# Kernel tuning notes

Measured on AMD Instinct MI355X. Metric: run time of the kernel, lower is better.

Reference implementation:

```python
import jax, jax.numpy as jnp
import numpy as np

N_HEADS = 8
D_MODEL = 256
HEAD_DEPTH = D_MODEL // N_HEADS
B, S = 2, 4096


def setup_inputs() -> dict:
    key = jax.random.key(0)
    ks = jax.random.split(key, 8)
    scale = 1.0 / np.sqrt(D_MODEL)
    return {
        "q": jax.random.normal(ks[0], (B, S, D_MODEL), dtype=jnp.float32),
        "k": jax.random.normal(ks[1], (B, S, D_MODEL), dtype=jnp.float32),
        "v": jax.random.normal(ks[2], (B, S, D_MODEL), dtype=jnp.float32),
        "mask": jax.random.randint(ks[3], (B, S, S), 0, 2).astype(jnp.bool_),
        "wq": jax.random.normal(ks[4], (D_MODEL, D_MODEL), dtype=jnp.float32) * scale,
        "wk": jax.random.normal(ks[5], (D_MODEL, D_MODEL), dtype=jnp.float32) * scale,
        "wv": jax.random.normal(ks[6], (D_MODEL, D_MODEL), dtype=jnp.float32) * scale,
        "w_out": jax.random.normal(ks[7], (D_MODEL, D_MODEL), dtype=jnp.float32) * scale,
    }


def _split_heads(x):
    # [B, S, D] -> [B, H, S, Dh]
    b, s, _ = x.shape
    return x.reshape(b, s, N_HEADS, HEAD_DEPTH).transpose(0, 2, 1, 3)


def reference(q, k, v, mask, wq, wk, wv, w_out):
    Q = _split_heads(q @ wq)
    K = _split_heads(k @ wk)
    V = _split_heads(v @ wv)
    # [B, H, Sq, Sk]
    scores = jnp.einsum('bhqd,bhkd->bhqk', Q, K) / jnp.sqrt(
        jnp.asarray(HEAD_DEPTH, dtype=Q.dtype))
    # mask True -> -inf, broadcast over heads
    scores = jnp.where(mask[:, None, :, :], -jnp.inf, scores)
    probs = jax.nn.softmax(scores, axis=-1)
    attn = jnp.einsum('bhqk,bhkd->bhqd', probs, V)
    attn = attn.transpose(0, 2, 1, 3).reshape(q.shape[0], -1, D_MODEL)
    return attn @ w_out
```

## Files before the change

### kernel.cpp

```cpp
#include <hip/hip_runtime.h>
#include <stdint.h>

typedef __bf16 bf16;
typedef __bf16 bf16x8 __attribute__((ext_vector_type(8)));
typedef __bf16 bf16x4 __attribute__((ext_vector_type(4)));
typedef float  f32x4  __attribute__((ext_vector_type(4)));
typedef float  f32x16 __attribute__((ext_vector_type(16)));
typedef float  float4v __attribute__((ext_vector_type(4)));
typedef unsigned int uint;
typedef unsigned long long ull;

#define QSCALE 0.25505003984214403f

__global__ __launch_bounds__(256) void transpose_w(
    const float* __restrict__ w0, const float* __restrict__ w1,
    const float* __restrict__ w2, const float* __restrict__ w3,
    bf16* __restrict__ WT) {
  const int wsel = blockIdx.z;
  const float* W = wsel == 0 ? w0 : wsel == 1 ? w1 : wsel == 2 ? w2 : w3;
  const int k0 = blockIdx.x * 64, n0 = blockIdx.y * 64;
  __shared__ __align__(16) bf16 t[64][72];
  const int tid = threadIdx.x;
  {
    const int kk = (tid >> 4) << 2;
    const int nn = (tid & 15) << 2;
#pragma unroll
    for (int r = 0; r < 4; ++r) {
      float4v a = *(const float4v*)(W + (size_t)(k0 + kk + r) * 256 + n0 + nn);
#pragma unroll
      for (int j = 0; j < 4; ++j) t[nn + j][kk + r] = (bf16)a[j];
    }
  }
  __syncthreads();
  {
    const int ni = tid >> 2;
    const int c  = (tid & 3) * 16;
    bf16x8 o0 = *(const bf16x8*)(&t[ni][c]);
    bf16x8 o1 = *(const bf16x8*)(&t[ni][c + 8]);
    bf16* dst = WT + (size_t)wsel * 65536 + (size_t)(n0 + ni) * 256 + k0 + c;
    *(bf16x8*)dst = o0;
    *(bf16x8*)(dst + 8) = o1;
  }
}

__global__ __launch_bounds__(256) void proj_pack(
    const float* __restrict__ xq, const float* __restrict__ xk, const float* __restrict__ xv,
    const bf16* __restrict__ WT,
    bf16* __restrict__ Qo, bf16* __restrict__ Ko, bf16* __restrict__ Vt,
    const int* __restrict__ mask, uint* __restrict__ M2) {
  const int tid = threadIdx.x;
  if (blockIdx.x >= 768) {
    const int pid = blockIdx.x - 768;
    const int wid = pid * 4 + (tid >> 6);
    const int lane = tid & 63;
    const int row = wid >> 2, chunk = wid & 3;
    const int b = row >> 12, q = row & 4095;
    const size_t base = (size_t)row * 4096 + chunk * 1024 + lane;
    ull bl[16];
#pragma unroll
    for (int j = 0; j < 16; ++j) bl[j] = __ballot(mask[base + 64 * j] != 0);
    if (lane == 0) {
      uint* o = M2 + (size_t)b * 524288 + q;
#pragma unroll
      for (int j = 0; j < 16; ++j) {
        const int kdw = chunk * 32 + 2 * j;
        o[(size_t)kdw * 4096] = (uint)bl[j];
        o[(size_t)(kdw + 1) * 4096] = (uint)(bl[j] >> 32);
      }
    }
    return;
  }
  const int z = blockIdx.x >> 8;
  const int r8 = blockIdx.x & 255;
  const int m0 = (r8 >> 1) * 64, n0 = (r8 & 1) * 128;
  const float* X = z == 0 ? xq : (z == 1 ? xk : xv);
  const bf16* wt = WT + (size_t)z * 65536;
  const int wave = tid >> 6, lane = tid & 63;
  const int nl = lane & 15, quad = lane >> 4;
  const int arow = m0 + wave * 16 + nl;
  const float* xrow = X + (size_t)arow * 256;

  f32x4 zero4 = {0.f, 0.f, 0.f, 0.f};
  f32x4 acc[8];
#pragma unroll
  for (int i = 0; i < 8; ++i) acc[i] = zero4;

  for (int ks = 0; ks < 8; ++ks) {
    float4v a0 = *(const float4v*)(xrow + ks * 32 + quad * 8);
    float4v a1 = *(const float4v*)(xrow + ks * 32 + quad * 8 + 4);
    bf16x8 af;
#pragma unroll
    for (int i = 0; i < 4; ++i) { af[i] = (bf16)a0[i]; af[4 + i] = (bf16)a1[i]; }
#pragma unroll
    for (int nf = 0; nf < 8; ++nf) {
      bf16x8 bfr = *(const bf16x8*)(wt + (size_t)(n0 + nf * 16 + nl) * 256 + ks * 32 + quad * 8);
      acc[nf] = __builtin_amdgcn_mfma_f32_16x16x32_bf16(af, bfr, acc[nf], 0, 0, 0);
    }
  }

  const int Rbase = m0 + wave * 16 + quad * 4;
  if (z == 2) {
    const int b = Rbase >> 12, s = Rbase & 4095;
#pragma unroll
    for (int nf = 0; nf < 8; ++nf) {
      const int col = n0 + nf * 16 + nl;
      const int h = col >> 5, d = col & 31;
      bf16x4 o;
#pragma unroll
      for (int rr = 0; rr < 4; ++rr) o[rr] = (bf16)acc[nf][rr];
      *(bf16x4*)(Vt + (((size_t)(b * 8 + h)) * 32 + d) * 4096 + s) = o;
    }
  } else {
    const float scale = (z == 0) ? QSCALE : 1.0f;
    bf16* Out = z == 0 ? Qo : Ko;
#pragma unroll
    for (int nf = 0; nf < 8; ++nf) {
      const int col = n0 + nf * 16 + nl;
      const int h = col >> 5, d = col & 31;
#pragma unroll
      for (int rr = 0; rr < 4; ++rr) {
        const int R = Rbase + rr;
        const int b = R >> 12, s = R & 4095;
        Out[(((size_t)(b * 8 + h)) * 4096 + s) * 32 + d] = (bf16)(acc[nf][rr] * scale);
      }
    }
  }
}

__global__ __launch_bounds__(256) void attn_kernel(
    const bf16* __restrict__ Qg, const bf16* __restrict__ Kg,
    const bf16* __restrict__ Vtg, const uint* __restrict__ M2,
    bf16* __restrict__ Og) {
  const int bh = blockIdx.y, b = bh >> 3, h = bh & 7;
  const int q0 = blockIdx.x * 64;
  const int tid = threadIdx.x, w = tid >> 6, lane = tid & 63;
  const int nl = lane & 31, half = lane >> 5;

  __shared__ float Ored[4][32][66];
  __shared__ float Lsum[64][8];

  bf16x8 qf[2][2];
  {
    const bf16* Qbase = Qg + ((size_t)bh * 4096 + q0) * 32;
#pragma unroll
    for (int qt = 0; qt < 2; ++qt)
#pragma unroll
      for (int s = 0; s < 2; ++s)
        qf[qt][s] = *(const bf16x8*)(Qbase + (size_t)(qt * 32 + nl) * 32 + s * 16 + half * 8);
  }

  const bf16* Kbase = Kg + (size_t)bh * 4096 * 32 + (size_t)(w * 32 + nl) * 32;
  const bf16* Vbase = Vtg + ((size_t)bh * 32 + nl) * 4096 + w * 32 + half * 4;
  const uint* Mbase = M2 + (size_t)b * 524288 + q0 + nl;

  f32x16 acc0, acc1;
#pragma unroll
  for (int i = 0; i < 16; ++i) { acc0[i] = 0.f; acc1[i] = 0.f; }
  float lsum0 = 0.f, lsum1 = 0.f;

  for (int kt = 0; kt < 32; ++kt) {
    const bf16* kc = Kbase + (size_t)kt * 4096;
    bf16x8 ka0 = *(const bf16x8*)(kc + half * 8);
    bf16x8 ka1 = *(const bf16x8*)(kc + 16 + half * 8);
    const bf16* vc = Vbase + (size_t)kt * 128;
    bf16x4 v00 = *(const bf16x4*)(vc);
    bf16x4 v01 = *(const bf16x4*)(vc + 8);
    bf16x4 v10 = *(const bf16x4*)(vc + 16);
    bf16x4 v11 = *(const bf16x4*)(vc + 24);
    bf16x8 va0, va1;
#pragma unroll
    for (int j = 0; j < 4; ++j) {
      va0[j] = v00[j]; va0[4 + j] = v01[j];
      va1[j] = v10[j]; va1[4 + j] = v11[j];
    }
    const uint* mp = Mbase + (size_t)(kt * 4 + w) * 4096;
    const int minv0 = (int)((~mp[0]) >> (4 * half));
    const int minv1 = (int)((~mp[32]) >> (4 * half));

    f32x16 z16;
#pragma unroll
    for (int i = 0; i < 16; ++i) z16[i] = 0.f;
    f32x16 st0 = __builtin_amdgcn_mfma_f32_32x32x16_bf16(ka0, qf[0][0], z16, 0, 0, 0);
    st0 = __builtin_amdgcn_mfma_f32_32x32x16_bf16(ka1, qf[0][1], st0, 0, 0, 0);
    f32x16 st1 = __builtin_amdgcn_mfma_f32_32x32x16_bf16(ka0, qf[1][0], z16, 0, 0, 0);
    st1 = __builtin_amdgcn_mfma_f32_32x32x16_bf16(ka1, qf[1][1], st1, 0, 0, 0);

    bf16 pe0[16], pe1[16];
#pragma unroll
    for (int g = 0; g < 4; ++g)
#pragma unroll
      for (int r = 0; r < 4; ++r) {
        const int i = g * 4 + r, off = r + 8 * g;
        float e0 = __builtin_amdgcn_exp2f(st0[i]);
        float e1 = __builtin_amdgcn_exp2f(st1[i]);
        const uint k0m = (uint)__builtin_amdgcn_sbfe(minv0, off, 1);
        const uint k1m = (uint)__builtin_amdgcn_sbfe(minv1, off, 1);
        e0 = __uint_as_float(__float_as_uint(e0) & k0m);
        e1 = __uint_as_float(__float_as_uint(e1) & k1m);
        lsum0 += e0; lsum1 += e1;
        pe0[i] = (bf16)e0; pe1[i] = (bf16)e1;
      }
    const bf16x8 pb00 = *(const bf16x8*)&pe0[0];
    const bf16x8 pb01 = *(const bf16x8*)&pe0[8];
    const bf16x8 pb10 = *(const bf16x8*)&pe1[0];
    const bf16x8 pb11 = *(const bf16x8*)&pe1[8];

    acc0 = __builtin_amdgcn_mfma_f32_32x32x16_bf16(va0, pb00, acc0, 0, 0, 0);
    acc0 = __builtin_amdgcn_mfma_f32_32x32x16_bf16(va1, pb01, acc0, 0, 0, 0);
    acc1 = __builtin_amdgcn_mfma_f32_32x32x16_bf16(va0, pb10, acc1, 0, 0, 0);
    acc1 = __builtin_amdgcn_mfma_f32_32x32x16_bf16(va1, pb11, acc1, 0, 0, 0);
  }

#pragma unroll
  for (int g = 0; g < 4; ++g)
#pragma unroll
    for (int r = 0; r < 4; ++r) {
      const int d = r + 8 * g + 4 * half, i = g * 4 + r;
      Ored[w][d][nl] = acc0[i];
      Ored[w][d][32 + nl] = acc1[i];
    }
  Lsum[nl][w * 2 + half] = lsum0;
  Lsum[32 + nl][w * 2 + half] = lsum1;
  __syncthreads();
  if (tid < 64) {
    float s = 0.f;
#pragma unroll
    for (int j = 0; j < 8; ++j) s += Lsum[tid][j];
    Lsum[tid][0] = 1.0f / s;
  }
  __syncthreads();
  {
    const int q = tid >> 2, db = (tid & 3) * 8;
    const float rl = Lsum[q][0];
    bf16x8 o;
#pragma unroll
    for (int dj = 0; dj < 8; ++dj) {
      const float s = Ored[0][db + dj][q] + Ored[1][db + dj][q] +
                      Ored[2][db + dj][q] + Ored[3][db + dj][q];
      o[dj] = (bf16)(s * rl);
    }
    *(bf16x8*)(Og + ((size_t)(b * 4096 + q0 + q)) * 256 + h * 32 + db) = o;
  }
}

__global__ __launch_bounds__(256) void gemm_out(
    const bf16* __restrict__ A, const bf16* __restrict__ WTo, float* __restrict__ C) {
  const int m0 = blockIdx.x * 64, n0 = blockIdx.y * 128;
  const int tid = threadIdx.x, wave = tid >> 6, lane = tid & 63;
  const int nl = lane & 15, quad = lane >> 4;
  const int arow = m0 + wave * 16 + nl;

  f32x4 zero4 = {0.f, 0.f, 0.f, 0.f};
  f32x4 acc[8];
#pragma unroll
  for (int i = 0; i < 8; ++i) acc[i] = zero4;

  for (int ks = 0; ks < 8; ++ks) {
    bf16x8 af = *(const bf16x8*)(A + (size_t)arow * 256 + ks * 32 + quad * 8);
#pragma unroll
    for (int nf = 0; nf < 8; ++nf) {
      bf16x8 bfr = *(const bf16x8*)(WTo + (size_t)(n0 + nf * 16 + nl) * 256 + ks * 32 + quad * 8);
      acc[nf] = __builtin_amdgcn_mfma_f32_16x16x32_bf16(af, bfr, acc[nf], 0, 0, 0);
    }
  }
  const int Rbase = m0 + wave * 16 + quad * 4;
#pragma unroll
  for (int nf = 0; nf < 8; ++nf)
#pragma unroll
    for (int r = 0; r < 4; ++r)
      C[(size_t)(Rbase + r) * 256 + n0 + nf * 16 + nl] = acc[nf][r];
}

extern "C" void kernel_launch(void* const* d_in, const int* in_sizes, int n_in,
                              void* d_out, int out_size, void* d_ws, size_t ws_size,
                              hipStream_t stream) {
  const float* q  = (const float*)d_in[0];
  const float* k  = (const float*)d_in[1];
  const float* v  = (const float*)d_in[2];
  const int*  mask = (const int*)d_in[3];
  const float* wq = (const float*)d_in[4];
  const float* wk = (const float*)d_in[5];
  const float* wv = (const float*)d_in[6];
  const float* wo = (const float*)d_in[7];
  float* out = (float*)d_out;

  uint8_t* ws = (uint8_t*)d_ws;
  bf16* WT = (bf16*)ws;
  bf16* Qb = (bf16*)(ws + (512u << 10));
  bf16* Kb = Qb + 2097152;
  bf16* Vt = Kb + 2097152;
  uint* Mb = (uint*)((uint8_t*)(Vt + 2097152));
  bf16* Ao = (bf16*)((uint8_t*)Mb + (4u << 20));

  transpose_w<<<dim3(4, 4, 4), 256, 0, stream>>>(wq, wk, wv, wo, WT);
  proj_pack<<<dim3(768 + 8192), 256, 0, stream>>>(q, k, v, WT, Qb, Kb, Vt, mask, Mb);
  attn_kernel<<<dim3(64, 16), 256, 0, stream>>>(Qb, Kb, Vt, Mb, Ao);
  gemm_out<<<dim3(128, 2), 256, 0, stream>>>(Ao, WT + 3 * 65536, out);
}
```

Baseline: 354.6 us.

## Pack Q/K/V into fragment-major layout, prefetch tiles, and remap blocks per XCD

The projection kernel now writes Q, K and V in a tiled layout that matches the MFMA fragment order. Each lane in the attention kernel can then load full contiguous 16-byte vectors instead of strided bf16x4 pieces that need reassembly. The attention loop is software-pipelined two-deep so the next key tile's K, V and mask loads are in flight during the current step. A 1D grid remaps blocks so each XCD works on the same batch-heads for L2 locality. The cost is more live registers for the prefetched fragments and scattered writes in the projection epilogue.

Result: faster. 329.7 us (-7.0%).

```diff
diff --git a/kernel.cpp b/kernel.cpp
--- a/kernel.cpp
+++ b/kernel.cpp
@@ -11,6 +11,7 @@
 typedef unsigned long long ull;
 
 #define QSCALE 0.25505003984214403f
+
 
 __global__ __launch_bounds__(256) void transpose_w(
     const float* __restrict__ w0, const float* __restrict__ w1,
@@ -46,7 +47,7 @@
 __global__ __launch_bounds__(256) void proj_pack(
     const float* __restrict__ xq, const float* __restrict__ xk, const float* __restrict__ xv,
     const bf16* __restrict__ WT,
-    bf16* __restrict__ Qo, bf16* __restrict__ Ko, bf16* __restrict__ Vt,
+    bf16* __restrict__ Qp, bf16* __restrict__ Kp, bf16* __restrict__ Vp,
     const int* __restrict__ mask, uint* __restrict__ M2) {
   const int tid = threadIdx.x;
   if (blockIdx.x >= 768) {
@@ -100,7 +101,10 @@
 
   const int Rbase = m0 + wave * 16 + quad * 4;
   if (z == 2) {
-    const int b = Rbase >> 12, s = Rbase & 4095;
+    const int b = Rbase >> 12, key = Rbase & 4095;
+    const int key5 = key & 31;
+    const int sub = ((key5 >> 4) << 1) | ((key5 >> 2) & 1);
+    const int g = (key5 >> 3) & 1;
 #pragma unroll
     for (int nf = 0; nf < 8; ++nf) {
       const int col = n0 + nf * 16 + nl;
@@ -108,82 +112,89 @@
       bf16x4 o;
 #pragma unroll
       for (int rr = 0; rr < 4; ++rr) o[rr] = (bf16)acc[nf][rr];
-      *(bf16x4*)(Vt + (((size_t)(b * 8 + h)) * 32 + d) * 4096 + s) = o;
+      const size_t off = (size_t)(b * 8 + h) * 131072 + (size_t)(key >> 5) * 1024 +
+                         sub * 256 + d * 8 + g * 4;
+      *(bf16x4*)(Vp + off) = o;
     }
   } else {
     const float scale = (z == 0) ? QSCALE : 1.0f;
-    bf16* Out = z == 0 ? Qo : Ko;
+    bf16* Out = z == 0 ? Qp : Kp;
 #pragma unroll
     for (int nf = 0; nf < 8; ++nf) {
       const int col = n0 + nf * 16 + nl;
       const int h = col >> 5, d = col & 31;
+      const int sub = d >> 3, j = d & 7;
 #pragma unroll
       for (int rr = 0; rr < 4; ++rr) {
         const int R = Rbase + rr;
-        const int b = R >> 12, s = R & 4095;
-        Out[(((size_t)(b * 8 + h)) * 4096 + s) * 32 + d] = (bf16)(acc[nf][rr] * scale);
+        const int b = R >> 12, sidx = R & 4095;
+        const size_t off = (size_t)(b * 8 + h) * 131072 + (size_t)(sidx >> 5) * 1024 +
+                           sub * 256 + (sidx & 31) * 8 + j;
+        Out[off] = (bf16)(acc[nf][rr] * scale);
       }
     }
   }
 }
 
 __global__ __launch_bounds__(256) void attn_kernel(
-    const bf16* __restrict__ Qg, const bf16* __restrict__ Kg,
-    const bf16* __restrict__ Vtg, const uint* __restrict__ M2,
+    const bf16* __restrict__ Qp, const bf16* __restrict__ Kp,
+    const bf16* __restrict__ Vp, const uint* __restrict__ M2,
     bf16* __restrict__ Og) {
-  const int bh = blockIdx.y, b = bh >> 3, h = bh & 7;
-  const int q0 = blockIdx.x * 64;
+  const int id = blockIdx.x;
+  const int xcd = id & 7, slot = id >> 3;
+  const int bh = xcd * 2 + (slot >> 6);
+  const int q0 = (slot & 63) * 64;
+  const int b = bh >> 3, h = bh & 7;
   const int tid = threadIdx.x, w = tid >> 6, lane = tid & 63;
   const int nl = lane & 31, half = lane >> 5;
 
   __shared__ float Ored[4][32][66];
   __shared__ float Lsum[64][8];
 
+  const size_t bhbase = (size_t)bh * 131072;
+  const int so0 = half * 256 + nl * 8;
+  const int so1 = 512 + half * 256 + nl * 8;
+
   bf16x8 qf[2][2];
-  {
-    const bf16* Qbase = Qg + ((size_t)bh * 4096 + q0) * 32;
-#pragma unroll
-    for (int qt = 0; qt < 2; ++qt)
-#pragma unroll
-      for (int s = 0; s < 2; ++s)
-        qf[qt][s] = *(const bf16x8*)(Qbase + (size_t)(qt * 32 + nl) * 32 + s * 16 + half * 8);
-  }
-
-  const bf16* Kbase = Kg + (size_t)bh * 4096 * 32 + (size_t)(w * 32 + nl) * 32;
-  const bf16* Vbase = Vtg + ((size_t)bh * 32 + nl) * 4096 + w * 32 + half * 4;
-  const uint* Mbase = M2 + (size_t)b * 524288 + q0 + nl;
-
-  f32x16 acc0, acc1;
-#pragma unroll
-  for (int i = 0; i < 16; ++i) { acc0[i] = 0.f; acc1[i] = 0.f; }
+#pragma unroll
+  for (int qt = 0; qt < 2; ++qt) {
+    const bf16* qb = Qp + bhbase + (size_t)((q0 >> 5) + qt) * 1024;
+    qf[qt][0] = *(const bf16x8*)(qb + so0);
+    qf[qt][1] = *(const bf16x8*)(qb + so1);
+  }
+
+  const bf16* Kw = Kp + bhbase + (size_t)w * 1024;
+  const bf16* Vw = Vp + bhbase + (size_t)w * 1024;
+  const uint* Mw = M2 + (size_t)b * 524288 + (size_t)w * 4096 + q0 + nl;
+
+  f32x16 z16;
+#pragma unroll
+  for (int i = 0; i < 16; ++i) z16[i] = 0.f;
+  f32x16 acc0 = z16, acc1 = z16;
   float lsum0 = 0.f, lsum1 = 0.f;
 
-  for (int kt = 0; kt < 32; ++kt) {
-    const bf16* kc = Kbase + (size_t)kt * 4096;
-    bf16x8 ka0 = *(const bf16x8*)(kc + half * 8);
-    bf16x8 ka1 = *(const bf16x8*)(kc + 16 + half * 8);
-    const bf16* vc = Vbase + (size_t)kt * 128;
-    bf16x4 v00 = *(const bf16x4*)(vc);
-    bf16x4 v01 = *(const bf16x4*)(vc + 8);
-    bf16x4 v10 = *(const bf16x4*)(vc + 16);
-    bf16x4 v11 = *(const bf16x4*)(vc + 24);
-    bf16x8 va0, va1;
-#pragma unroll
-    for (int j = 0; j < 4; ++j) {
-      va0[j] = v00[j]; va0[4 + j] = v01[j];
-      va1[j] = v10[j]; va1[4 + j] = v11[j];
-    }
-    const uint* mp = Mbase + (size_t)(kt * 4 + w) * 4096;
-    const int minv0 = (int)((~mp[0]) >> (4 * half));
-    const int minv1 = (int)((~mp[32]) >> (4 * half));
-
-    f32x16 z16;
-#pragma unroll
-    for (int i = 0; i < 16; ++i) z16[i] = 0.f;
-    f32x16 st0 = __builtin_amdgcn_mfma_f32_32x32x16_bf16(ka0, qf[0][0], z16, 0, 0, 0);
-    st0 = __builtin_amdgcn_mfma_f32_32x32x16_bf16(ka1, qf[0][1], st0, 0, 0, 0);
-    f32x16 st1 = __builtin_amdgcn_mfma_f32_32x32x16_bf16(ka0, qf[1][0], z16, 0, 0, 0);
-    st1 = __builtin_amdgcn_mfma_f32_32x32x16_bf16(ka1, qf[1][1], st1, 0, 0, 0);
+  struct Frag { bf16x8 ka0, ka1, va0, va1; uint m0, m1; };
+  auto LOADF = [&](int kt) -> Frag {
+    Frag f;
+    const bf16* kc = Kw + (size_t)kt * 4096;
+    const bf16* vc = Vw + (size_t)kt * 4096;
+    f.ka0 = *(const bf16x8*)(kc + so0);
+    f.ka1 = *(const bf16x8*)(kc + so1);
+    f.va0 = *(const bf16x8*)(vc + so0);
+    f.va1 = *(const bf16x8*)(vc + so1);
+    const uint* mp = Mw + (size_t)kt * 16384;
+    f.m0 = mp[0];
+    f.m1 = mp[32];
+    return f;
+  };
+
+  auto STEP = [&](const Frag& f) {
+    const int minv0 = (int)((~f.m0) >> (4 * half));
+    const int minv1 = (int)((~f.m1) >> (4 * half));
+    f32x16 st0 = __builtin_amdgcn_mfma_f32_32x32x16_bf16(f.ka0, qf[0][0], z16, 0, 0, 0);
+    st0 = __builtin_amdgcn_mfma_f32_32x32x16_bf16(f.ka1, qf[0][1], st0, 0, 0, 0);
+    f32x16 st1 = __builtin_amdgcn_mfma_f32_32x32x16_bf16(f.ka0, qf[1][0], z16, 0, 0, 0);
+    st1 = __builtin_amdgcn_mfma_f32_32x32x16_bf16(f.ka1, qf[1][1], st1, 0, 0, 0);
 
     bf16 pe0[16], pe1[16];
 #pragma unroll
@@ -205,10 +216,18 @@
     const bf16x8 pb10 = *(const bf16x8*)&pe1[0];
     const bf16x8 pb11 = *(const bf16x8*)&pe1[8];
 
-    acc0 = __builtin_amdgcn_mfma_f32_32x32x16_bf16(va0, pb00, acc0, 0, 0, 0);
-    acc0 = __builtin_amdgcn_mfma_f32_32x32x16_bf16(va1, pb01, acc0, 0, 0, 0);
-    acc1 = __builtin_amdgcn_mfma_f32_32x32x16_bf16(va0, pb10, acc1, 0, 0, 0);
-    acc1 = __builtin_amdgcn_mfma_f32_32x32x16_bf16(va1, pb11, acc1, 0, 0, 0);
+    acc0 = __builtin_amdgcn_mfma_f32_32x32x16_bf16(f.va0, pb00, acc0, 0, 0, 0);
+    acc0 = __builtin_amdgcn_mfma_f32_32x32x16_bf16(f.va1, pb01, acc0, 0, 0, 0);
+    acc1 = __builtin_amdgcn_mfma_f32_32x32x16_bf16(f.va0, pb10, acc1, 0, 0, 0);
+    acc1 = __builtin_amdgcn_mfma_f32_32x32x16_bf16(f.va1, pb11, acc1, 0, 0, 0);
+  };
+
+  Frag fa = LOADF(0), fb;
+  for (int kt = 0; kt < 32; kt += 2) {
+    fb = LOADF(kt + 1);
+    STEP(fa);
+    if (kt + 2 < 32) fa = LOADF(kt + 2);
+    STEP(fb);
   }
 
 #pragma unroll
@@ -286,14 +305,14 @@
 
   uint8_t* ws = (uint8_t*)d_ws;
   bf16* WT = (bf16*)ws;
-  bf16* Qb = (bf16*)(ws + (512u << 10));
-  bf16* Kb = Qb + 2097152;
-  bf16* Vt = Kb + 2097152;
-  uint* Mb = (uint*)((uint8_t*)(Vt + 2097152));
+  bf16* Qp = (bf16*)(ws + (512u << 10));
+  bf16* Kp = Qp + 2097152;
+  bf16* Vp = Kp + 2097152;
+  uint* Mb = (uint*)((uint8_t*)(Vp + 2097152));
   bf16* Ao = (bf16*)((uint8_t*)Mb + (4u << 20));
 
   transpose_w<<<dim3(4, 4, 4), 256, 0, stream>>>(wq, wk, wv, wo, WT);
-  proj_pack<<<dim3(768 + 8192), 256, 0, stream>>>(q, k, v, WT, Qb, Kb, Vt, mask, Mb);
-  attn_kernel<<<dim3(64, 16), 256, 0, stream>>>(Qb, Kb, Vt, Mb, Ao);
+  proj_pack<<<dim3(768 + 8192), 256, 0, stream>>>(q, k, v, WT, Qp, Kp, Vp, mask, Mb);
+  attn_kernel<<<dim3(1024), 256, 0, stream>>>(Qp, Kp, Vp, Mb, Ao);
   gemm_out<<<dim3(128, 2), 256, 0, stream>>>(Ao, WT + 3 * 65536, out);
 }
```
